# Kernel optimization log

Measured on AMD Instinct MI355X. Metric: run time of the kernel, lower is better.

The kernel has to match this reference:

```python
import jax, jax.numpy as jnp
from jax import lax
import numpy as np

B, IN_DIM, T, L, CONN = 32, 256, 512, 512, 256
LN_EPS = 1e-3  # keras LayerNormalization default


def setup_inputs() -> dict:
    key = jax.random.key(0)
    ks = jax.random.split(key, 16)
    g = lambda k, shape, fan: jax.random.normal(k, shape, jnp.float32) * (2.0 / sum(fan)) ** 0.5
    return {
        "x": jax.random.normal(ks[0], (B, IN_DIM, T), jnp.float32),
        "connectivity": jax.random.normal(ks[1], (B, T, CONN), jnp.float32),
        # RandomFourierFeatures: trainable projection + bias, layer-normalized cos features
        "Wf": g(ks[2], (IN_DIM, L), (IN_DIM, L)),
        "bf": jax.random.uniform(ks[3], (L,), jnp.float32, 0.0, 2.0 * np.pi),
        "gamma": jnp.ones((L,), jnp.float32),
        "beta": jnp.zeros((L,), jnp.float32),
        # input gate
        "Wi": g(ks[4], (L, L), (L, L)),
        "Ri": g(ks[5], (L, L), (L, L)),
        "bi": jnp.zeros((L,), jnp.float32),
        # forget gate
        "Wg": g(ks[6], (L, L), (L, L)),
        "Rg": g(ks[7], (L, L), (L, L)),
        "bg": jnp.zeros((L,), jnp.float32),
        # connectivity Dense projection
        "Wc": g(ks[8], (CONN, L), (CONN, L)),
        "bc": jnp.zeros((L,), jnp.float32),
        # learned initial states (stored squeezed to [L])
        "init_h": g(ks[9], (L,), (1, L)),
        "init_c": g(ks[10], (L,), (1, L)),
    }


def reference(x, connectivity, Wf, bf, gamma, beta, Wi, Ri, bi, Wg, Rg, bg, Wc, bc, init_h, init_c):
    xt = jnp.transpose(x, (0, 2, 1))                      # [B, T, in_dim]
    # random fourier features with layer normalization
    p = jnp.cos(xt @ Wf + bf)                             # [B, T, L]
    mu = jnp.mean(p, axis=-1, keepdims=True)
    var = jnp.var(p, axis=-1, keepdims=True)
    z = gamma * (p - mu) * lax.rsqrt(var + LN_EPS) + beta

    o = jnp.sin(z)                                        # sinusoid output gate
    u = connectivity @ Wc + bc                            # [B, T, L] connectivity injection

    b = x.shape[0]
    # hidden_states[t+1] = z_t in the original, so the recurrent term at step t is z_{t-1}
    h0 = jnp.broadcast_to(init_h, (b, 1, z.shape[-1]))
    z_prev = jnp.concatenate([h0, z[:, :-1, :]], axis=1)  # [B, T, L]

    i = jax.nn.sigmoid(z @ Wi + z_prev @ Ri + bi)
    f = jax.nn.sigmoid(z @ Wg + z_prev @ Rg + bg)
    iu = i * u

    def step(c, fi):
        ft, iut = fi
        c = ft * c + iut
        return c, c

    c0 = jnp.broadcast_to(init_c, (b, z.shape[-1]))
    _, cs = lax.scan(step, c0, (jnp.moveaxis(f, 1, 0), jnp.moveaxis(iu, 1, 0)))
    cs = jnp.moveaxis(cs, 0, 1)                           # [B, T, L]
    h = o * cs
    return jnp.transpose(h, (0, 2, 1))                    # [B, L, T]
```

## Files before the change

kernel.cpp:

```cpp
#include <hip/hip_runtime.h>
#include <hip/hip_bf16.h>

#define NB 32
#define IN_DIM 256
#define NT 512
#define NL 512
#define NCONN 256
#define LN_EPS 1e-3f
#define M_TOT (NB * NT)

typedef __attribute__((ext_vector_type(8))) short short8;
typedef __attribute__((ext_vector_type(4))) float f32x4;

__device__ __forceinline__ void async_copy16(void* lds_dst, const void* g_src) {
    __builtin_amdgcn_global_load_lds(
        (const __attribute__((address_space(1))) unsigned int*)g_src,
        (__attribute__((address_space(3))) unsigned int*)lds_dst, 16, 0, 0);
}

__global__ __launch_bounds__(256) void xprep_transpose(
    const float* __restrict__ x, __hip_bfloat16* __restrict__ Axt)
{
    __shared__ float t[64][65];
    const int tilesPerB = (IN_DIM / 64) * (NT / 64);
    const int b  = blockIdx.x / tilesPerB;
    const int tl = blockIdx.x % tilesPerB;
    const int k0 = (tl / (NT / 64)) * 64;
    const int t0 = (tl % (NT / 64)) * 64;
    const int tid = threadIdx.x;
    const float* src = x + (size_t)b * IN_DIM * NT;
    for (int idx = tid; idx < 4096; idx += 256) {
        const int kk = idx >> 6, tt = idx & 63;
        t[kk][tt] = src[(size_t)(k0 + kk) * NT + t0 + tt];
    }
    __syncthreads();
    for (int idx = tid; idx < 4096; idx += 256) {
        const int tt = idx >> 6, kk = idx & 63;
        Axt[((size_t)b * NT + t0 + tt) * IN_DIM + k0 + kk] =
            __float2bfloat16(t[kk][tt]);
    }
}

__global__ void fill_init_h(const float* __restrict__ init_h,
                            __hip_bfloat16* __restrict__ abuf)
{
    const int l = threadIdx.x;
    const __hip_bfloat16 v = __float2bfloat16(init_h[l]);
    for (int b = 0; b < NB; b++)
        abuf[((size_t)b * NT) * 1024 + 512 + l] = v;
}

__global__ __launch_bounds__(512, 2) void k1_mfma_fourier_ln(
    const __hip_bfloat16* __restrict__ Axt,
    const __hip_bfloat16* __restrict__ WfT,
    const float* __restrict__ bf, const float* __restrict__ gamma,
    const float* __restrict__ beta,
    __hip_bfloat16* __restrict__ abuf)
{
    constexpr int ABYTES = 64 * 128;
    constexpr int BBYTES = 512 * 128;
    constexpr int NBUFB  = ABYTES + BBYTES;
    __shared__ __align__(16) char lds[2 * NBUFB];
    __shared__ float pS[64][8], pQ[64][8];
    __shared__ float mS[64], rS[64];

    const int tid  = threadIdx.x;
    const int wave = tid >> 6, lane = tid & 63;
    const int m0 = blockIdx.x * 64;

    f32x4 acc[4][4];
#pragma unroll
    for (int mi = 0; mi < 4; mi++)
#pragma unroll
        for (int ni = 0; ni < 4; ni++) acc[mi][ni] = f32x4{0.f, 0.f, 0.f, 0.f};

    const int rowq = tid >> 3;
    const int sswz = ((tid & 7) ^ (rowq & 7)) << 4;
    const char* Ab = (const char*)Axt;
    const char* Bb = (const char*)WfT;

    auto stage = [&](int buf, int kt) {
        const size_t kb = (size_t)kt * 128;
        char* base = lds + buf * NBUFB;
        async_copy16(base + tid * 16,
                     Ab + (size_t)(m0 + rowq) * 512 + kb + sswz);
#pragma unroll
        for (int j = 0; j < 8; j++) {
            const int row = j * 64 + rowq;
            async_copy16(base + ABYTES + (j * 512 + tid) * 16,
                         Bb + (size_t)row * 512 + kb + sswz);
        }
    };

    const int l15 = lane & 15, lq = lane >> 4, l7 = lane & 7;
    int kxB[2];
#pragma unroll
    for (int ks = 0; ks < 2; ks++) kxB[ks] = ((ks * 4 + lq) ^ l7) << 4;

    stage(0, 0);
    int cur = 0;
#pragma unroll 1
    for (int kt = 0; kt < 4; kt++) {
        __syncthreads();
        if (kt + 1 < 4) stage(cur ^ 1, kt + 1);
        const char* sA = lds + cur * NBUFB;
        const char* sB = sA + ABYTES;
#pragma unroll
        for (int ks = 0; ks < 2; ks++) {
            const int kx = kxB[ks];
            short8 a[4], b[4];
#pragma unroll
            for (int mi = 0; mi < 4; mi++)
                a[mi] = *(const short8*)(sA + (size_t)(mi * 16 + l15) * 128 + kx);
#pragma unroll
            for (int ni = 0; ni < 4; ni++)
                b[ni] = *(const short8*)(sB +
                    (size_t)(wave * 64 + ni * 16 + l15) * 128 + kx);
#pragma unroll
            for (int ni = 0; ni < 4; ni++)
#pragma unroll
                for (int mi = 0; mi < 4; mi++)
                    acc[mi][ni] = __builtin_amdgcn_mfma_f32_16x16x32_bf16(
                        a[mi], b[ni], acc[mi][ni], 0, 0, 0);
        }
        cur ^= 1;
    }

    int cg[4]; float bfc[4];
#pragma unroll
    for (int ni = 0; ni < 4; ni++) {
        cg[ni] = wave * 64 + ni * 16 + l15;
        bfc[ni] = bf[cg[ni]];
    }

#pragma unroll
    for (int mi = 0; mi < 4; mi++) {
#pragma unroll
        for (int r = 0; r < 4; r++) {
            float s = 0.f, q = 0.f;
#pragma unroll
            for (int ni = 0; ni < 4; ni++) {
                const float p = __cosf(acc[mi][ni][r] + bfc[ni]);
                s += p; q += p * p;
            }
#pragma unroll
            for (int off = 8; off >= 1; off >>= 1) {
                s += __shfl_xor(s, off);
                q += __shfl_xor(q, off);
            }
            if (l15 == 0) {
                const int row = mi * 16 + lq * 4 + r;
                pS[row][wave] = s;
                pQ[row][wave] = q;
            }
        }
    }
    __syncthreads();
    if (tid < 64) {
        float a = 0.f, qq = 0.f;
#pragma unroll
        for (int w = 0; w < 8; w++) { a += pS[tid][w]; qq += pQ[tid][w]; }
        const float mu = a * (1.0f / NL);
        const float var = qq * (1.0f / NL) - mu * mu;
        mS[tid] = mu;
        rS[tid] = rsqrtf(var + LN_EPS);
    }
    __syncthreads();

    float gm[4], bt[4];
#pragma unroll
    for (int ni = 0; ni < 4; ni++) { gm[ni] = gamma[cg[ni]]; bt[ni] = beta[cg[ni]]; }

#pragma unroll
    for (int mi = 0; mi < 4; mi++) {
#pragma unroll
        for (int r = 0; r < 4; r++) {
            const int row = mi * 16 + lq * 4 + r;
            const int m = m0 + row;
            const int t = m & (NT - 1);
            const float mu = mS[row], rs = rS[row];
#pragma unroll
            for (int ni = 0; ni < 4; ni++) {
                const float p = __cosf(acc[mi][ni][r] + bfc[ni]);
                const float z = gm[ni] * (p - mu) * rs + bt[ni];
                const __hip_bfloat16 zb = __float2bfloat16(z);
                abuf[(size_t)m * 1024 + cg[ni]] = zb;
                if (t != NT - 1) abuf[(size_t)(m + 1) * 1024 + 512 + cg[ni]] = zb;
            }
        }
    }
}

__global__ __launch_bounds__(256) void wconv_transpose(
    const float* __restrict__ src, __hip_bfloat16* __restrict__ dst,
    int K, int N, int lddst, int k_off)
{
    __shared__ float t[64][65];
    const int ntn = N >> 6;
    const int k0 = (blockIdx.x / ntn) << 6;
    const int n0 = (blockIdx.x % ntn) << 6;
    const int tid = threadIdx.x;
    for (int idx = tid; idx < 4096; idx += 256) {
        const int kk = idx >> 6, nn = idx & 63;
        t[kk][nn] = src[(size_t)(k0 + kk) * N + n0 + nn];
    }
    __syncthreads();
    for (int idx = tid; idx < 4096; idx += 256) {
        const int nn = idx >> 6, kk = idx & 63;
        dst[(size_t)(n0 + nn) * lddst + k_off + k0 + kk] = __float2bfloat16(t[kk][nn]);
    }
}

__global__ __launch_bounds__(256) void conv_bf16_vec(
    const float* __restrict__ src, __hip_bfloat16* __restrict__ dst, int n)
{
    const int e = (blockIdx.x * 256 + threadIdx.x) * 4;
    if (e < n) {
        const float4 v = *(const float4*)(src + e);
        dst[e + 0] = __float2bfloat16(v.x);
        dst[e + 1] = __float2bfloat16(v.y);
        dst[e + 2] = __float2bfloat16(v.z);
        dst[e + 3] = __float2bfloat16(v.w);
    }
}

template<int KTOT, bool DUAL>
__global__ __launch_bounds__(512, 2) void gemm_mfma(
    const __hip_bfloat16* __restrict__ A,
    const __hip_bfloat16* __restrict__ B0,
    const __hip_bfloat16* __restrict__ B1,
    const float* __restrict__ bi, const float* __restrict__ bg,
    const float* __restrict__ bc,
    __hip_bfloat16* __restrict__ fb, __hip_bfloat16* __restrict__ ub)
{
    constexpr int ABYTES = 256 * 128;
    constexpr int BBYTES = 128 * 128;
    constexpr int NBUFB  = ABYTES + (DUAL ? 2 : 1) * BBYTES;
    __shared__ __align__(16) char lds[2 * NBUFB];

    const int tid  = threadIdx.x;
    const int wave = tid >> 6, lane = tid & 63;
    const int wm = wave >> 1, wn = wave & 1;
    const int m0 = blockIdx.x * 256;
    const int n0 = blockIdx.y * 128;

    f32x4 acc0[4][4];
    f32x4 acc1[DUAL ? 4 : 1][DUAL ? 4 : 1];
#pragma unroll
    for (int mi = 0; mi < 4; mi++)
#pragma unroll
        for (int ni = 0; ni < 4; ni++) {
            acc0[mi][ni] = f32x4{0.f, 0.f, 0.f, 0.f};
            if constexpr (DUAL) acc1[mi][ni] = f32x4{0.f, 0.f, 0.f, 0.f};
        }

    const int rowq = tid >> 3;
    const int sswz = (((tid & 7) ^ (rowq & 7)) << 4);
    const char* Ab  = (const char*)A;
    const char* B0b = (const char*)B0;
    const char* B1b = (const char*)B1;
    constexpr size_t ldk = (size_t)KTOT * 2;

    auto stage = [&](int buf, int kt) {
        const size_t kb = (size_t)kt * 128;
        char* base = lds + buf * NBUFB;
#pragma unroll
        for (int j = 0; j < 4; j++) {
            const int row = j * 64 + rowq;
            async_copy16(base + (j * 512 + tid) * 16,
                         Ab + (size_t)(m0 + row) * ldk + kb + sswz);
        }
#pragma unroll
        for (int j = 0; j < 2; j++) {
            const int row = j * 64 + rowq;
            async_copy16(base + ABYTES + (j * 512 + tid) * 16,
                         B0b + (size_t)(n0 + row) * ldk + kb + sswz);
            if constexpr (DUAL)
                async_copy16(base + ABYTES + BBYTES + (j * 512 + tid) * 16,
                             B1b + (size_t)(n0 + row) * ldk + kb + sswz);
        }
    };

    const int l15 = lane & 15, lq = lane >> 4, l7 = lane & 7;
    int kxB[2];
#pragma unroll
    for (int ks = 0; ks < 2; ks++) kxB[ks] = ((ks * 4 + lq) ^ l7) << 4;

    constexpr int KSTEPS = KTOT / 64;
    stage(0, 0);
    int cur = 0;
#pragma unroll 1
    for (int kt = 0; kt < KSTEPS; kt++) {
        __syncthreads();
        if (kt + 1 < KSTEPS) stage(cur ^ 1, kt + 1);
        const char* sA  = lds + cur * NBUFB;
        const char* sB0 = sA + ABYTES;
        const char* sB1 = sB0 + BBYTES;
#pragma unroll
        for (int ks = 0; ks < 2; ks++) {
            const int kx = kxB[ks];
            short8 a[4], b0[4];
#pragma unroll
            for (int mi = 0; mi < 4; mi++)
                a[mi] = *(const short8*)(sA +
                    (size_t)(wm * 64 + mi * 16 + l15) * 128 + kx);
#pragma unroll
            for (int ni = 0; ni < 4; ni++)
                b0[ni] = *(const short8*)(sB0 +
                    (size_t)(wn * 64 + ni * 16 + l15) * 128 + kx);
#pragma unroll
            for (int ni = 0; ni < 4; ni++)
#pragma unroll
                for (int mi = 0; mi < 4; mi++)
                    acc0[mi][ni] = __builtin_amdgcn_mfma_f32_16x16x32_bf16(
                        a[mi], b0[ni], acc0[mi][ni], 0, 0, 0);
            if constexpr (DUAL) {
                short8 b1[4];
#pragma unroll
                for (int ni = 0; ni < 4; ni++)
                    b1[ni] = *(const short8*)(sB1 +
                        (size_t)(wn * 64 + ni * 16 + l15) * 128 + kx);
#pragma unroll
                for (int ni = 0; ni < 4; ni++)
#pragma unroll
                    for (int mi = 0; mi < 4; mi++)
                        acc1[mi][ni] = __builtin_amdgcn_mfma_f32_16x16x32_bf16(
                            a[mi], b1[ni], acc1[mi][ni], 0, 0, 0);
            }
        }
        cur ^= 1;
    }

#pragma unroll
    for (int ni = 0; ni < 4; ni++) {
        const int l = n0 + wn * 64 + ni * 16 + l15;
        float bil = 0.f, bgl = 0.f, bcl = 0.f;
        if constexpr (DUAL) { bil = bi[l]; bgl = bg[l]; }
        else                { bcl = bc[l]; }
#pragma unroll
        for (int mi = 0; mi < 4; mi++) {
#pragma unroll
            for (int r = 0; r < 4; r++) {
                const int m = m0 + wm * 64 + mi * 16 + lq * 4 + r;
                const size_t idx = (size_t)m * NL + l;
                if constexpr (DUAL) {
                    const float ipre = acc0[mi][ni][r] + bil;
                    const float fpre = acc1[mi][ni][r] + bgl;
                    const float fv = 1.f / (1.f + __expf(-fpre));
                    const float iv = 1.f / (1.f + __expf(-ipre));
                    const float uv = __bfloat162float(ub[idx]);
                    fb[idx] = __float2bfloat16(fv);
                    ub[idx] = __float2bfloat16(iv * uv);
                } else {
                    ub[idx] = __float2bfloat16(acc0[mi][ni][r] + bcl);
                }
            }
        }
    }
}

__global__ __launch_bounds__(64) void k3_scan(
    const __hip_bfloat16* __restrict__ zab,
    const __hip_bfloat16* __restrict__ fb,
    const __hip_bfloat16* __restrict__ ub,
    const float* __restrict__ init_c, float* __restrict__ out)
{
    const int b = blockIdx.x >> 3;
    const int l = ((blockIdx.x & 7) << 6) + threadIdx.x;
    float c = init_c[l];

    const __hip_bfloat16* zp = zab + (size_t)b * NT * 1024 + l;
    const __hip_bfloat16* fp = fb  + (size_t)b * NT * NL + l;
    const __hip_bfloat16* ip = ub  + (size_t)b * NT * NL + l;
    float* op = out + ((size_t)b * NL + l) * NT;

    for (int t0 = 0; t0 < NT; t0 += 16) {
        float fv[16], iv[16], zv[16];
#pragma unroll
        for (int j = 0; j < 16; j++) {
            fv[j] = __bfloat162float(fp[(size_t)(t0 + j) * NL]);
            iv[j] = __bfloat162float(ip[(size_t)(t0 + j) * NL]);
            zv[j] = __bfloat162float(zp[(size_t)(t0 + j) * 1024]);
        }
        float h[16];
#pragma unroll
        for (int j = 0; j < 16; j++) {
            c = fv[j] * c + iv[j];
            h[j] = __sinf(zv[j]) * c;
        }
        float4* o4 = (float4*)(op + t0);
        o4[0] = make_float4(h[0],  h[1],  h[2],  h[3]);
        o4[1] = make_float4(h[4],  h[5],  h[6],  h[7]);
        o4[2] = make_float4(h[8],  h[9],  h[10], h[11]);
        o4[3] = make_float4(h[12], h[13], h[14], h[15]);
    }
}

extern "C" void kernel_launch(void* const* d_in, const int* in_sizes, int n_in,
                              void* d_out, int out_size, void* d_ws, size_t ws_size,
                              hipStream_t stream)
{
    const float* x      = (const float*)d_in[0];
    const float* conn   = (const float*)d_in[1];
    const float* Wf     = (const float*)d_in[2];
    const float* bfv    = (const float*)d_in[3];
    const float* gamma  = (const float*)d_in[4];
    const float* beta   = (const float*)d_in[5];
    const float* Wi     = (const float*)d_in[6];
    const float* Ri     = (const float*)d_in[7];
    const float* bi     = (const float*)d_in[8];
    const float* Wg     = (const float*)d_in[9];
    const float* Rg     = (const float*)d_in[10];
    const float* bg     = (const float*)d_in[11];
    const float* Wc     = (const float*)d_in[12];
    const float* bc     = (const float*)d_in[13];
    const float* init_h = (const float*)d_in[14];
    const float* init_c = (const float*)d_in[15];

    char* w = (char*)d_ws;
    __hip_bfloat16* abuf = (__hip_bfloat16*)w;  w += (size_t)M_TOT * 1024 * 2;
    __hip_bfloat16* cbuf = (__hip_bfloat16*)w;  w += (size_t)M_TOT * NCONN * 2;
    __hip_bfloat16* fbuf = (__hip_bfloat16*)w;  w += (size_t)M_TOT * NL * 2;
    __hip_bfloat16* ubuf = (__hip_bfloat16*)w;  w += (size_t)M_TOT * NL * 2;
    __hip_bfloat16* xbuf = (__hip_bfloat16*)w;  w += (size_t)M_TOT * IN_DIM * 2;
    __hip_bfloat16* WfT  = (__hip_bfloat16*)w;  w += (size_t)NL * IN_DIM * 2;
    __hip_bfloat16* Bti  = (__hip_bfloat16*)w;  w += (size_t)NL * 1024 * 2;
    __hip_bfloat16* Btg  = (__hip_bfloat16*)w;  w += (size_t)NL * 1024 * 2;
    __hip_bfloat16* Btc  = (__hip_bfloat16*)w;  w += (size_t)NL * NCONN * 2;

    wconv_transpose<<<32, 256, 0, stream>>>(Wf, WfT, 256, 512, 256, 0);
    wconv_transpose<<<64, 256, 0, stream>>>(Wi, Bti, 512, 512, 1024, 0);
    wconv_transpose<<<64, 256, 0, stream>>>(Ri, Bti, 512, 512, 1024, 512);
    wconv_transpose<<<64, 256, 0, stream>>>(Wg, Btg, 512, 512, 1024, 0);
    wconv_transpose<<<64, 256, 0, stream>>>(Rg, Btg, 512, 512, 1024, 512);
    wconv_transpose<<<32, 256, 0, stream>>>(Wc, Btc, 256, 512, 256, 0);
    conv_bf16_vec<<<(M_TOT * NCONN / 4 + 255) / 256, 256, 0, stream>>>(
        conn, cbuf, M_TOT * NCONN);
    xprep_transpose<<<NB * 32, 256, 0, stream>>>(x, xbuf);
    fill_init_h<<<1, 512, 0, stream>>>(init_h, abuf);

    k1_mfma_fourier_ln<<<M_TOT / 64, 512, 0, stream>>>(
        xbuf, WfT, bfv, gamma, beta, abuf);

    gemm_mfma<NCONN, false><<<dim3(M_TOT / 256, NL / 128), 512, 0, stream>>>(
        cbuf, Btc, nullptr, nullptr, nullptr, bc, nullptr, ubuf);

    gemm_mfma<1024, true><<<dim3(M_TOT / 256, NL / 128), 512, 0, stream>>>(
        abuf, Bti, Btg, bi, bg, nullptr, fbuf, ubuf);

    k3_scan<<<NB * 8, 64, 0, stream>>>(abuf, fbuf, ubuf, init_c, (float*)d_out);
}
```

Baseline: 145.6 us.

## Use a 4-slot K=32 LDS ring with vmcnt-based waits in GEMMs

Replaces the double-buffered 64-wide K stage with a four-slot ring of 32-wide K slices. Three slices are prefetched, and each step waits with an explicit s_waitcnt vmcnt count plus a raw s_barrier instead of a full __syncthreads, so more global loads stay in flight. It also moves to a 1D grid with a block-index remap that groups tiles across M and N, changing L2 locality, and uses a new LDS swizzle for the narrower rows. The hand-counted vmcnt values and the slot-reuse timing are fragile: a wrong count could read stale LDS data.

Result: no change. 142.8 us (-2.0%).

```diff
diff --git a/kernel.cpp b/kernel.cpp
--- a/kernel.cpp
+++ b/kernel.cpp
@@ -225,7 +225,7 @@
 }
 
 template<int KTOT, bool DUAL>
-__global__ __launch_bounds__(512, 2) void gemm_mfma(
+__global__ __launch_bounds__(512, 2) void gemm_pipe(
     const __hip_bfloat16* __restrict__ A,
     const __hip_bfloat16* __restrict__ B0,
     const __hip_bfloat16* __restrict__ B1,
@@ -233,16 +233,20 @@
     const float* __restrict__ bc,
     __hip_bfloat16* __restrict__ fb, __hip_bfloat16* __restrict__ ub)
 {
-    constexpr int ABYTES = 256 * 128;
-    constexpr int BBYTES = 128 * 128;
-    constexpr int NBUFB  = ABYTES + (DUAL ? 2 : 1) * BBYTES;
-    __shared__ __align__(16) char lds[2 * NBUFB];
+    constexpr int H = KTOT / 32;
+    constexpr int A_SLOT = 256 * 32 * 2;
+    constexpr int B_SLOT = 128 * 32 * 2;
+    constexpr int A_TOT  = 4 * A_SLOT;
+    constexpr int B_TOT  = 4 * B_SLOT;
+    __shared__ __align__(16) char lds[A_TOT + (DUAL ? 2 : 1) * B_TOT];
 
     const int tid  = threadIdx.x;
     const int wave = tid >> 6, lane = tid & 63;
     const int wm = wave >> 1, wn = wave & 1;
-    const int m0 = blockIdx.x * 256;
-    const int n0 = blockIdx.y * 128;
+    const int d = blockIdx.x;
+    const int L = ((d & 7) << 5) | (d >> 3);
+    const int m0 = (L >> 2) << 8;
+    const int n0 = (L & 3) << 7;
 
     f32x4 acc0[4][4];
     f32x4 acc1[DUAL ? 4 : 1][DUAL ? 4 : 1];
@@ -254,82 +258,93 @@
             if constexpr (DUAL) acc1[mi][ni] = f32x4{0.f, 0.f, 0.f, 0.f};
         }
 
-    const int rowq = tid >> 3;
-    const int sswz = (((tid & 7) ^ (rowq & 7)) << 4);
     const char* Ab  = (const char*)A;
     const char* B0b = (const char*)B0;
     const char* B1b = (const char*)B1;
     constexpr size_t ldk = (size_t)KTOT * 2;
 
-    auto stage = [&](int buf, int kt) {
-        const size_t kb = (size_t)kt * 128;
-        char* base = lds + buf * NBUFB;
-#pragma unroll
-        for (int j = 0; j < 4; j++) {
-            const int row = j * 64 + rowq;
-            async_copy16(base + (j * 512 + tid) * 16,
-                         Ab + (size_t)(m0 + row) * ldk + kb + sswz);
-        }
+    const int rA0 = tid >> 2;
+    const int slotT = tid & 3;
+    const int l15 = lane & 15, lq = lane >> 4;
+    const int pb = ((lq ^ ((l15 >> 1) & 3)) << 4);
+    int aOff[4], bOff[4];
+#pragma unroll
+    for (int mi = 0; mi < 4; mi++) aOff[mi] = (wm * 64 + mi * 16 + l15) * 64 + pb;
+#pragma unroll
+    for (int ni = 0; ni < 4; ni++) bOff[ni] = (wn * 64 + ni * 16 + l15) * 64 + pb;
+
+    auto stageHalf = [&](int h) {
+        const int slot = h & 3;
+        const size_t kb = (size_t)h * 64;
+        char* aBase  = lds + slot * A_SLOT;
+        char* b0Base = lds + A_TOT + slot * B_SLOT;
 #pragma unroll
         for (int j = 0; j < 2; j++) {
-            const int row = j * 64 + rowq;
-            async_copy16(base + ABYTES + (j * 512 + tid) * 16,
-                         B0b + (size_t)(n0 + row) * ldk + kb + sswz);
-            if constexpr (DUAL)
-                async_copy16(base + ABYTES + BBYTES + (j * 512 + tid) * 16,
-                             B1b + (size_t)(n0 + row) * ldk + kb + sswz);
-        }
+            const int r = j * 128 + rA0;
+            const int lsl = slotT ^ ((r >> 1) & 3);
+            async_copy16(aBase + j * 8192 + tid * 16,
+                         Ab + (size_t)(m0 + r) * ldk + kb + lsl * 16);
+        }
+        const int rB = rA0;
+        const int lslB = slotT ^ ((rB >> 1) & 3);
+        async_copy16(b0Base + tid * 16,
+                     B0b + (size_t)(n0 + rB) * ldk + kb + lslB * 16);
+        if constexpr (DUAL)
+            async_copy16(b0Base + B_TOT + tid * 16,
+                         B1b + (size_t)(n0 + rB) * ldk + kb + lslB * 16);
     };
 
-    const int l15 = lane & 15, lq = lane >> 4, l7 = lane & 7;
-    int kxB[2];
-#pragma unroll
-    for (int ks = 0; ks < 2; ks++) kxB[ks] = ((ks * 4 + lq) ^ l7) << 4;
-
-    constexpr int KSTEPS = KTOT / 64;
-    stage(0, 0);
-    int cur = 0;
-#pragma unroll 1
-    for (int kt = 0; kt < KSTEPS; kt++) {
-        __syncthreads();
-        if (kt + 1 < KSTEPS) stage(cur ^ 1, kt + 1);
-        const char* sA  = lds + cur * NBUFB;
-        const char* sB0 = sA + ABYTES;
-        const char* sB1 = sB0 + BBYTES;
-#pragma unroll
-        for (int ks = 0; ks < 2; ks++) {
-            const int kx = kxB[ks];
-            short8 a[4], b0[4];
+    auto computeHalf = [&](int h) {
+        const char* sA  = lds + (h & 3) * A_SLOT;
+        const char* sB0 = lds + A_TOT + (h & 3) * B_SLOT;
+        short8 a[4], b0[4];
+#pragma unroll
+        for (int mi = 0; mi < 4; mi++)
+            a[mi] = *(const short8*)(sA + aOff[mi]);
+#pragma unroll
+        for (int ni = 0; ni < 4; ni++)
+            b0[ni] = *(const short8*)(sB0 + bOff[ni]);
+#pragma unroll
+        for (int ni = 0; ni < 4; ni++)
 #pragma unroll
             for (int mi = 0; mi < 4; mi++)
-                a[mi] = *(const short8*)(sA +
-                    (size_t)(wm * 64 + mi * 16 + l15) * 128 + kx);
+                acc0[mi][ni] = __builtin_amdgcn_mfma_f32_16x16x32_bf16(
+                    a[mi], b0[ni], acc0[mi][ni], 0, 0, 0);
+        if constexpr (DUAL) {
+            const char* sB1 = sB0 + B_TOT;
+            short8 b1[4];
 #pragma unroll
             for (int ni = 0; ni < 4; ni++)
-                b0[ni] = *(const short8*)(sB0 +
-                    (size_t)(wn * 64 + ni * 16 + l15) * 128 + kx);
+                b1[ni] = *(const short8*)(sB1 + bOff[ni]);
 #pragma unroll
             for (int ni = 0; ni < 4; ni++)
 #pragma unroll
                 for (int mi = 0; mi < 4; mi++)
-                    acc0[mi][ni] = __builtin_amdgcn_mfma_f32_16x16x32_bf16(
-                        a[mi], b0[ni], acc0[mi][ni], 0, 0, 0);
-            if constexpr (DUAL) {
-                short8 b1[4];
-#pragma unroll
-                for (int ni = 0; ni < 4; ni++)
-                    b1[ni] = *(const short8*)(sB1 +
-                        (size_t)(wn * 64 + ni * 16 + l15) * 128 + kx);
-#pragma unroll
-                for (int ni = 0; ni < 4; ni++)
-#pragma unroll
-                    for (int mi = 0; mi < 4; mi++)
-                        acc1[mi][ni] = __builtin_amdgcn_mfma_f32_16x16x32_bf16(
-                            a[mi], b1[ni], acc1[mi][ni], 0, 0, 0);
-            }
-        }
-        cur ^= 1;
-    }
+                    acc1[mi][ni] = __builtin_amdgcn_mfma_f32_16x16x32_bf16(
+                        a[mi], b1[ni], acc1[mi][ni], 0, 0, 0);
+        }
+    };
+
+    stageHalf(0); stageHalf(1); stageHalf(2);
+
+#pragma unroll 4
+    for (int h = 0; h < H - 2; h++) {
+        if constexpr (DUAL) asm volatile("s_waitcnt vmcnt(8)" ::: "memory");
+        else                asm volatile("s_waitcnt vmcnt(6)" ::: "memory");
+        __builtin_amdgcn_s_barrier();
+        __builtin_amdgcn_sched_barrier(0);
+        if (h + 3 < H) stageHalf(h + 3);
+        computeHalf(h);
+    }
+    if constexpr (DUAL) asm volatile("s_waitcnt vmcnt(4)" ::: "memory");
+    else                asm volatile("s_waitcnt vmcnt(3)" ::: "memory");
+    __builtin_amdgcn_s_barrier();
+    __builtin_amdgcn_sched_barrier(0);
+    computeHalf(H - 2);
+    asm volatile("s_waitcnt vmcnt(0)" ::: "memory");
+    __builtin_amdgcn_s_barrier();
+    __builtin_amdgcn_sched_barrier(0);
+    computeHalf(H - 1);
 
 #pragma unroll
     for (int ni = 0; ni < 4; ni++) {
@@ -442,10 +457,10 @@
     k1_mfma_fourier_ln<<<M_TOT / 64, 512, 0, stream>>>(
         xbuf, WfT, bfv, gamma, beta, abuf);
 
-    gemm_mfma<NCONN, false><<<dim3(M_TOT / 256, NL / 128), 512, 0, stream>>>(
+    gemm_pipe<NCONN, false><<<256, 512, 0, stream>>>(
         cbuf, Btc, nullptr, nullptr, nullptr, bc, nullptr, ubuf);
 
-    gemm_mfma<1024, true><<<dim3(M_TOT / 256, NL / 128), 512, 0, stream>>>(
+    gemm_pipe<1024, true><<<256, 512, 0, stream>>>(
         abuf, Bti, Btg, bi, bg, nullptr, fbuf, ubuf);
 
     k3_scan<<<NB * 8, 64, 0, stream>>>(abuf, fbuf, ubuf, init_c, (float*)d_out);
```

## Store z once and gather shifted rows in GEMM; merge gate weights into single 128x128 GEMM

Applied to the files above, without the earlier changes.

The Fourier/LN kernel now writes z once into a 512-wide buffer instead of writing it twice into a 1024-wide [z, z_prev] buffer. The gate GEMM builds the z_prev half of its A tile on the fly by loading row m-1, or init_h at t=0. The input and forget gate weights are stacked into one 1024x1024 B matrix, and the dual-B 256x128 tile kernel is replaced by a single-B 128x128 tile kernel with 256 threads. Blocks are swizzled across 8 groups so that blocks sharing data run close together. This roughly halves the z write traffic and the workspace size. In exchange, A tiles are re-read per N tile, each block computes one gate and the other gate's tiles reload the same A rows, and the epilogue branches per column.

Measured after the change: 135.3 us. -7.1%, faster.

```diff
diff --git a/kernel.cpp b/kernel.cpp
--- a/kernel.cpp
+++ b/kernel.cpp
@@ -41,13 +41,11 @@
     }
 }
 
-__global__ void fill_init_h(const float* __restrict__ init_h,
-                            __hip_bfloat16* __restrict__ abuf)
+__global__ void fill_ihb(const float* __restrict__ init_h,
+                         __hip_bfloat16* __restrict__ ihb)
 {
     const int l = threadIdx.x;
-    const __hip_bfloat16 v = __float2bfloat16(init_h[l]);
-    for (int b = 0; b < NB; b++)
-        abuf[((size_t)b * NT) * 1024 + 512 + l] = v;
+    ihb[l] = __float2bfloat16(init_h[l]);
 }
 
 __global__ __launch_bounds__(512, 2) void k1_mfma_fourier_ln(
@@ -55,7 +53,7 @@
     const __hip_bfloat16* __restrict__ WfT,
     const float* __restrict__ bf, const float* __restrict__ gamma,
     const float* __restrict__ beta,
-    __hip_bfloat16* __restrict__ abuf)
+    __hip_bfloat16* __restrict__ zb)
 {
     constexpr int ABYTES = 64 * 128;
     constexpr int BBYTES = 512 * 128;
@@ -177,15 +175,12 @@
         for (int r = 0; r < 4; r++) {
             const int row = mi * 16 + lq * 4 + r;
             const int m = m0 + row;
-            const int t = m & (NT - 1);
             const float mu = mS[row], rs = rS[row];
 #pragma unroll
             for (int ni = 0; ni < 4; ni++) {
                 const float p = __cosf(acc[mi][ni][r] + bfc[ni]);
                 const float z = gm[ni] * (p - mu) * rs + bt[ni];
-                const __hip_bfloat16 zb = __float2bfloat16(z);
-                abuf[(size_t)m * 1024 + cg[ni]] = zb;
-                if (t != NT - 1) abuf[(size_t)(m + 1) * 1024 + 512 + cg[ni]] = zb;
+                zb[(size_t)m * 512 + cg[ni]] = __float2bfloat16(z);
             }
         }
     }
@@ -224,143 +219,141 @@
     }
 }
 
-template<int KTOT, bool DUAL>
-__global__ __launch_bounds__(512, 2) void gemm_mfma(
+template<int KTOT, int EPI>
+__global__ __launch_bounds__(256, 2) void gemm128(
     const __hip_bfloat16* __restrict__ A,
-    const __hip_bfloat16* __restrict__ B0,
-    const __hip_bfloat16* __restrict__ B1,
+    const __hip_bfloat16* __restrict__ B,
+    const __hip_bfloat16* __restrict__ ihb,
     const float* __restrict__ bi, const float* __restrict__ bg,
     const float* __restrict__ bc,
     __hip_bfloat16* __restrict__ fb, __hip_bfloat16* __restrict__ ub)
 {
-    constexpr int ABYTES = 256 * 128;
-    constexpr int BBYTES = 128 * 128;
-    constexpr int NBUFB  = ABYTES + (DUAL ? 2 : 1) * BBYTES;
-    __shared__ __align__(16) char lds[2 * NBUFB];
+    constexpr int NTN = (EPI == 1) ? 8 : 4;
+    constexpr int TB  = KTOT / 64;
+    __shared__ __align__(16) char lds[2][32768];
 
     const int tid  = threadIdx.x;
     const int wave = tid >> 6, lane = tid & 63;
     const int wm = wave >> 1, wn = wave & 1;
-    const int m0 = blockIdx.x * 256;
-    const int n0 = blockIdx.y * 128;
-
-    f32x4 acc0[4][4];
-    f32x4 acc1[DUAL ? 4 : 1][DUAL ? 4 : 1];
+    constexpr int CPX = 128 * NTN / 8;
+    const int d = blockIdx.x;
+    const int L = (d & 7) * CPX + (d >> 3);
+    const int m0 = (L / NTN) << 7;
+    const int n0 = (L % NTN) << 7;
+
+    f32x4 acc[4][4];
 #pragma unroll
     for (int mi = 0; mi < 4; mi++)
 #pragma unroll
-        for (int ni = 0; ni < 4; ni++) {
-            acc0[mi][ni] = f32x4{0.f, 0.f, 0.f, 0.f};
-            if constexpr (DUAL) acc1[mi][ni] = f32x4{0.f, 0.f, 0.f, 0.f};
-        }
-
-    const int rowq = tid >> 3;
-    const int sswz = (((tid & 7) ^ (rowq & 7)) << 4);
-    const char* Ab  = (const char*)A;
-    const char* B0b = (const char*)B0;
-    const char* B1b = (const char*)B1;
-    constexpr size_t ldk = (size_t)KTOT * 2;
+        for (int ni = 0; ni < 4; ni++) acc[mi][ni] = f32x4{0.f, 0.f, 0.f, 0.f};
 
     auto stage = [&](int buf, int kt) {
-        const size_t kb = (size_t)kt * 128;
-        char* base = lds + buf * NBUFB;
+        char* base = &lds[buf][0];
 #pragma unroll
         for (int j = 0; j < 4; j++) {
-            const int row = j * 64 + rowq;
-            async_copy16(base + (j * 512 + tid) * 16,
-                         Ab + (size_t)(m0 + row) * ldk + kb + sswz);
-        }
-#pragma unroll
-        for (int j = 0; j < 2; j++) {
-            const int row = j * 64 + rowq;
-            async_copy16(base + ABYTES + (j * 512 + tid) * 16,
-                         B0b + (size_t)(n0 + row) * ldk + kb + sswz);
-            if constexpr (DUAL)
-                async_copy16(base + ABYTES + BBYTES + (j * 512 + tid) * 16,
-                             B1b + (size_t)(n0 + row) * ldk + kb + sswz);
+            const int i = j * 256 + tid;
+            const int r = i >> 3;
+            const int sl = (i & 7) ^ (r & 7);
+            const int ke = kt * 64 + sl * 8;
+            const __hip_bfloat16* srcA;
+            if constexpr (EPI == 1) {
+                const int m = m0 + r;
+                if (ke < 512) {
+                    srcA = A + (size_t)m * 512 + ke;
+                } else {
+                    const int k2 = ke - 512;
+                    srcA = ((m & (NT - 1)) == 0) ? (ihb + k2)
+                                                 : (A + (size_t)(m - 1) * 512 + k2);
+                }
+            } else {
+                srcA = A + (size_t)(m0 + r) * KTOT + ke;
+            }
+            async_copy16(base + i * 16, srcA);
+            async_copy16(base + 16384 + i * 16,
+                         B + (size_t)(n0 + r) * KTOT + ke);
         }
     };
 
     const int l15 = lane & 15, lq = lane >> 4, l7 = lane & 7;
-    int kxB[2];
-#pragma unroll
-    for (int ks = 0; ks < 2; ks++) kxB[ks] = ((ks * 4 + lq) ^ l7) << 4;
-
-    constexpr int KSTEPS = KTOT / 64;
+    int kx[2];
+#pragma unroll
+    for (int ks = 0; ks < 2; ks++) kx[ks] = ((ks * 4 + lq) ^ l7) << 4;
+
     stage(0, 0);
     int cur = 0;
 #pragma unroll 1
-    for (int kt = 0; kt < KSTEPS; kt++) {
+    for (int kt = 0; kt < TB; kt++) {
         __syncthreads();
-        if (kt + 1 < KSTEPS) stage(cur ^ 1, kt + 1);
-        const char* sA  = lds + cur * NBUFB;
-        const char* sB0 = sA + ABYTES;
-        const char* sB1 = sB0 + BBYTES;
+        if (kt + 1 < TB) stage(cur ^ 1, kt + 1);
+        const char* sA = &lds[cur][0];
+        const char* sB = &lds[cur][16384];
 #pragma unroll
         for (int ks = 0; ks < 2; ks++) {
-            const int kx = kxB[ks];
-            short8 a[4], b0[4];
+            short8 a[4], b[4];
 #pragma unroll
             for (int mi = 0; mi < 4; mi++)
                 a[mi] = *(const short8*)(sA +
-                    (size_t)(wm * 64 + mi * 16 + l15) * 128 + kx);
+                    (size_t)(wm * 64 + mi * 16 + l15) * 128 + kx[ks]);
 #pragma unroll
             for (int ni = 0; ni < 4; ni++)
-                b0[ni] = *(const short8*)(sB0 +
-                    (size_t)(wn * 64 + ni * 16 + l15) * 128 + kx);
+                b[ni] = *(const short8*)(sB +
+                    (size_t)(wn * 64 + ni * 16 + l15) * 128 + kx[ks]);
 #pragma unroll
             for (int ni = 0; ni < 4; ni++)
 #pragma unroll
                 for (int mi = 0; mi < 4; mi++)
-                    acc0[mi][ni] = __builtin_amdgcn_mfma_f32_16x16x32_bf16(
-                        a[mi], b0[ni], acc0[mi][ni], 0, 0, 0);
-            if constexpr (DUAL) {
-                short8 b1[4];
-#pragma unroll
-                for (int ni = 0; ni < 4; ni++)
-                    b1[ni] = *(const short8*)(sB1 +
-                        (size_t)(wn * 64 + ni * 16 + l15) * 128 + kx);
-#pragma unroll
-                for (int ni = 0; ni < 4; ni++)
-#pragma unroll
-                    for (int mi = 0; mi < 4; mi++)
-                        acc1[mi][ni] = __builtin_amdgcn_mfma_f32_16x16x32_bf16(
-                            a[mi], b1[ni], acc1[mi][ni], 0, 0, 0);
-            }
+                    acc[mi][ni] = __builtin_amdgcn_mfma_f32_16x16x32_bf16(
+                        a[mi], b[ni], acc[mi][ni], 0, 0, 0);
         }
         cur ^= 1;
     }
 
 #pragma unroll
     for (int ni = 0; ni < 4; ni++) {
-        const int l = n0 + wn * 64 + ni * 16 + l15;
-        float bil = 0.f, bgl = 0.f, bcl = 0.f;
-        if constexpr (DUAL) { bil = bi[l]; bgl = bg[l]; }
-        else                { bcl = bc[l]; }
-#pragma unroll
-        for (int mi = 0; mi < 4; mi++) {
-#pragma unroll
-            for (int r = 0; r < 4; r++) {
-                const int m = m0 + wm * 64 + mi * 16 + lq * 4 + r;
-                const size_t idx = (size_t)m * NL + l;
-                if constexpr (DUAL) {
-                    const float ipre = acc0[mi][ni][r] + bil;
-                    const float fpre = acc1[mi][ni][r] + bgl;
-                    const float fv = 1.f / (1.f + __expf(-fpre));
-                    const float iv = 1.f / (1.f + __expf(-ipre));
-                    const float uv = __bfloat162float(ub[idx]);
-                    fb[idx] = __float2bfloat16(fv);
-                    ub[idx] = __float2bfloat16(iv * uv);
-                } else {
-                    ub[idx] = __float2bfloat16(acc0[mi][ni][r] + bcl);
+        const int gcol = n0 + wn * 64 + ni * 16 + l15;
+        if constexpr (EPI == 0) {
+            const float bcl = bc[gcol];
+#pragma unroll
+            for (int mi = 0; mi < 4; mi++)
+#pragma unroll
+                for (int r = 0; r < 4; r++) {
+                    const int m = m0 + wm * 64 + mi * 16 + lq * 4 + r;
+                    ub[(size_t)m * 512 + gcol] =
+                        __float2bfloat16(acc[mi][ni][r] + bcl);
                 }
+        } else {
+            if (gcol < 512) {
+                const float bil = bi[gcol];
+#pragma unroll
+                for (int mi = 0; mi < 4; mi++)
+#pragma unroll
+                    for (int r = 0; r < 4; r++) {
+                        const int m = m0 + wm * 64 + mi * 16 + lq * 4 + r;
+                        const size_t idx = (size_t)m * 512 + gcol;
+                        const float iv =
+                            1.f / (1.f + __expf(-(acc[mi][ni][r] + bil)));
+                        const float uv = __bfloat162float(ub[idx]);
+                        ub[idx] = __float2bfloat16(iv * uv);
+                    }
+            } else {
+                const int l2 = gcol - 512;
+                const float bgl = bg[l2];
+#pragma unroll
+                for (int mi = 0; mi < 4; mi++)
+#pragma unroll
+                    for (int r = 0; r < 4; r++) {
+                        const int m = m0 + wm * 64 + mi * 16 + lq * 4 + r;
+                        const float fv =
+                            1.f / (1.f + __expf(-(acc[mi][ni][r] + bgl)));
+                        fb[(size_t)m * 512 + l2] = __float2bfloat16(fv);
+                    }
             }
         }
     }
 }
 
 __global__ __launch_bounds__(64) void k3_scan(
-    const __hip_bfloat16* __restrict__ zab,
+    const __hip_bfloat16* __restrict__ zb,
     const __hip_bfloat16* __restrict__ fb,
     const __hip_bfloat16* __restrict__ ub,
     const float* __restrict__ init_c, float* __restrict__ out)
@@ -369,9 +362,9 @@
     const int l = ((blockIdx.x & 7) << 6) + threadIdx.x;
     float c = init_c[l];
 
-    const __hip_bfloat16* zp = zab + (size_t)b * NT * 1024 + l;
-    const __hip_bfloat16* fp = fb  + (size_t)b * NT * NL + l;
-    const __hip_bfloat16* ip = ub  + (size_t)b * NT * NL + l;
+    const __hip_bfloat16* zp = zb + (size_t)b * NT * 512 + l;
+    const __hip_bfloat16* fp = fb + (size_t)b * NT * NL + l;
+    const __hip_bfloat16* ip = ub + (size_t)b * NT * NL + l;
     float* op = out + ((size_t)b * NL + l) * NT;
 
     for (int t0 = 0; t0 < NT; t0 += 16) {
@@ -380,7 +373,7 @@
         for (int j = 0; j < 16; j++) {
             fv[j] = __bfloat162float(fp[(size_t)(t0 + j) * NL]);
             iv[j] = __bfloat162float(ip[(size_t)(t0 + j) * NL]);
-            zv[j] = __bfloat162float(zp[(size_t)(t0 + j) * 1024]);
+            zv[j] = __bfloat162float(zp[(size_t)(t0 + j) * 512]);
         }
         float h[16];
 #pragma unroll
@@ -418,35 +411,35 @@
     const float* init_c = (const float*)d_in[15];
 
     char* w = (char*)d_ws;
-    __hip_bfloat16* abuf = (__hip_bfloat16*)w;  w += (size_t)M_TOT * 1024 * 2;
+    __hip_bfloat16* zbuf = (__hip_bfloat16*)w;  w += (size_t)M_TOT * 512 * 2;
     __hip_bfloat16* cbuf = (__hip_bfloat16*)w;  w += (size_t)M_TOT * NCONN * 2;
     __hip_bfloat16* fbuf = (__hip_bfloat16*)w;  w += (size_t)M_TOT * NL * 2;
     __hip_bfloat16* ubuf = (__hip_bfloat16*)w;  w += (size_t)M_TOT * NL * 2;
     __hip_bfloat16* xbuf = (__hip_bfloat16*)w;  w += (size_t)M_TOT * IN_DIM * 2;
     __hip_bfloat16* WfT  = (__hip_bfloat16*)w;  w += (size_t)NL * IN_DIM * 2;
-    __hip_bfloat16* Bti  = (__hip_bfloat16*)w;  w += (size_t)NL * 1024 * 2;
-    __hip_bfloat16* Btg  = (__hip_bfloat16*)w;  w += (size_t)NL * 1024 * 2;
+    __hip_bfloat16* Btig = (__hip_bfloat16*)w;  w += (size_t)1024 * 1024 * 2;
     __hip_bfloat16* Btc  = (__hip_bfloat16*)w;  w += (size_t)NL * NCONN * 2;
+    __hip_bfloat16* ihb  = (__hip_bfloat16*)w;  w += 512 * 2;
 
     wconv_transpose<<<32, 256, 0, stream>>>(Wf, WfT, 256, 512, 256, 0);
-    wconv_transpose<<<64, 256, 0, stream>>>(Wi, Bti, 512, 512, 1024, 0);
-    wconv_transpose<<<64, 256, 0, stream>>>(Ri, Bti, 512, 512, 1024, 512);
-    wconv_transpose<<<64, 256, 0, stream>>>(Wg, Btg, 512, 512, 1024, 0);
-    wconv_transpose<<<64, 256, 0, stream>>>(Rg, Btg, 512, 512, 1024, 512);
+    wconv_transpose<<<64, 256, 0, stream>>>(Wi, Btig, 512, 512, 1024, 0);
+    wconv_transpose<<<64, 256, 0, stream>>>(Ri, Btig, 512, 512, 1024, 512);
+    wconv_transpose<<<64, 256, 0, stream>>>(Wg, Btig + (size_t)512 * 1024, 512, 512, 1024, 0);
+    wconv_transpose<<<64, 256, 0, stream>>>(Rg, Btig + (size_t)512 * 1024, 512, 512, 1024, 512);
     wconv_transpose<<<32, 256, 0, stream>>>(Wc, Btc, 256, 512, 256, 0);
     conv_bf16_vec<<<(M_TOT * NCONN / 4 + 255) / 256, 256, 0, stream>>>(
         conn, cbuf, M_TOT * NCONN);
     xprep_transpose<<<NB * 32, 256, 0, stream>>>(x, xbuf);
-    fill_init_h<<<1, 512, 0, stream>>>(init_h, abuf);
+    fill_ihb<<<1, 512, 0, stream>>>(init_h, ihb);
 
     k1_mfma_fourier_ln<<<M_TOT / 64, 512, 0, stream>>>(
-        xbuf, WfT, bfv, gamma, beta, abuf);
-
-    gemm_mfma<NCONN, false><<<dim3(M_TOT / 256, NL / 128), 512, 0, stream>>>(
+        xbuf, WfT, bfv, gamma, beta, zbuf);
+
+    gemm128<NCONN, 0><<<M_TOT / 128 * 4, 256, 0, stream>>>(
         cbuf, Btc, nullptr, nullptr, nullptr, bc, nullptr, ubuf);
 
-    gemm_mfma<1024, true><<<dim3(M_TOT / 256, NL / 128), 512, 0, stream>>>(
-        abuf, Bti, Btg, bi, bg, nullptr, fbuf, ubuf);
-
-    k3_scan<<<NB * 8, 64, 0, stream>>>(abuf, fbuf, ubuf, init_c, (float*)d_out);
-}
+    gemm128<1024, 1><<<M_TOT / 128 * 8, 256, 0, stream>>>(
+        zbuf, Btig, ihb, bi, bg, nullptr, fbuf, ubuf);
+
+    k3_scan<<<NB * 8, 64, 0, stream>>>(zbuf, fbuf, ubuf, init_c, (float*)d_out);
+}
```
